# Kernel optimization log

Measured on AMD Instinct MI355X. Metric: run time of the kernel, lower is better.

Reference implementation:

```python
import jax, jax.numpy as jnp
import numpy as np

# dims
B, NO, NE = 32, 100, 600          # batch, img objects, img edges
NK, KE, L = 1000, 1000, 8         # kg entities, kg edges, token len
R = 8                              # reasoning-program nodes
H, IMG, LOC = 512, 2048, 5        # hidden, img feat, loc feat
EMB, V, MID, C = 300, 10000, 512, 3000
PAD = 1


def lang_encode(tokens, embed, W, b):
    # masked mean-pool of word embeddings + projection (LanguageEncoder)
    m = (tokens != PAD).astype(jnp.float32)            # [B,N,L]
    e = embed[tokens]                                   # [B,N,L,EMB]
    pooled = (e * m[..., None]).sum(-2) / jnp.maximum(m.sum(-1, keepdims=True), 1.0)
    return jnp.tanh(pooled @ W + b)                     # [B,N,H]


def find_attn(q, k, mask, Wq, Wk, v):
    # Find module: additive attention of program-node queries over key set
    qp = q @ Wq                                         # [B,R,MID]
    kp = k @ Wk                                         # [B,N,MID]
    s = jnp.einsum('brnm,m->brn', jnp.tanh(qp[:, :, None, :] + kp[:, None, :, :]), v)
    if mask is not None:
        s = jnp.where(mask[:, None, :], s, -1e9)
    return jax.nn.softmax(s, axis=-1)                   # [B,R,N] attention maps


def setup_inputs():
    key = jax.random.key(0)
    ks = jax.random.split(key, 30)
    w = lambda i, shp: jax.random.normal(ks[i], shp, jnp.float32) * 0.05
    inp = {
        'img_feat': jax.random.normal(ks[0], (B, NO, IMG), jnp.float32),
        'img_loc': jax.random.uniform(ks[1], (B, NO, LOC), jnp.float32),
        'img_node1_id_list': jax.random.randint(ks[2], (B, NE), 0, NO),
        'img_node2_id_list': jax.random.randint(ks[3], (B, NE), 0, NO),
        'kg_entity': jax.random.randint(ks[4], (B, NK, L), 0, V),
        'kg_e1_ids_list': jax.random.randint(ks[5], (B, KE), 0, NK),
        'kg_e2_ids_list': jax.random.randint(ks[6], (B, KE), 0, NK),
        'kg_edge': jax.random.randint(ks[7], (B, KE, L), 0, V),
        'r_nodes': jax.random.randint(ks[8], (B, R, L), 0, V),
        'r_connects': jax.random.randint(ks[9], (B, R), 0, R),
        'r_type': jax.random.randint(ks[10], (B, R), 0, 3),
        'embed': w(11, (V, EMB)),
        'W_lang': w(12, (EMB, H)), 'b_lang': jnp.zeros((H,), jnp.float32),
        'W_img': w(13, (IMG, H)), 'b_img': jnp.zeros((H,), jnp.float32),
        'W_loc': w(14, (LOC, H)), 'b_loc': jnp.zeros((H,), jnp.float32),
        'W_rel': w(15, (2 * H, H)), 'b_rel': jnp.zeros((H,), jnp.float32),
        'Wq_n': w(16, (H, MID)), 'Wk_n': w(17, (H, MID)), 'v_n': w(18, (MID,)),
        'Wq_e': w(19, (H, MID)), 'Wk_e': w(20, (H, MID)), 'v_e': w(21, (MID,)),
        'W1': w(22, (H, MID)), 'b1': jnp.zeros((MID,), jnp.float32),
        'W2': w(23, (MID, C)), 'b2': jnp.zeros((C,), jnp.float32),
    }
    return inp


def reference(img_feat, img_loc, img_node1_id_list, img_node2_id_list, kg_entity,
              kg_e1_ids_list, kg_e2_ids_list, kg_edge, r_nodes, r_connects, r_type,
              embed, W_lang, b_lang, W_img, b_img, W_loc, b_loc, W_rel, b_rel,
              Wq_n, Wk_n, v_n, Wq_e, Wk_e, v_e, W1, b1, W2, b2):
    # --- image graph features ---
    img_f = img_feat @ W_img + b_img                    # [B,NO,H]
    img_node_feat = img_f + (img_loc @ W_loc + b_loc)
    n1 = jnp.take_along_axis(img_f, img_node1_id_list[..., None], axis=1)  # [B,NE,H]
    n2 = jnp.take_along_axis(img_f, img_node2_id_list[..., None], axis=1)
    img_edge_feat = jnp.concatenate([n1, n2], -1) @ W_rel + b_rel          # [B,NE,H]
    # --- kg graph features ---
    kg_node_feat = lang_encode(kg_entity, embed, W_lang, b_lang)           # [B,NK,H]
    kg_node_mask = jnp.any(kg_entity != PAD, axis=-1)                      # [B,NK]
    kg_edge_feat = lang_encode(kg_edge, embed, W_lang, b_lang)             # [B,KE,H]
    # --- reasoning-program node features ---
    r_feat = lang_encode(r_nodes, embed, W_lang, b_lang)                   # [B,R,H]
    # --- Find over nodes (img + kg entities) ---
    node_keys = jnp.concatenate([img_node_feat, kg_node_feat], axis=1)     # [B,NO+NK,H]
    node_mask = jnp.concatenate([jnp.ones((B, NO), bool), kg_node_mask], axis=1)
    all_map = find_attn(r_feat, node_keys, node_mask, Wq_n, Wk_n, v_n)     # [B,R,NO+NK]
    node_re = jnp.einsum('brn,bnh->brh', all_map, node_keys)               # grounded node feats
    # --- Find over edges (img + kg relations) ---
    edge_keys = jnp.concatenate([img_edge_feat, kg_edge_feat], axis=1)     # [B,NE+KE,H]
    edge_map = find_attn(r_feat, edge_keys, None, Wq_e, Wk_e, v_e)
    edge_ctx = jnp.einsum('brn,bnh->brh', edge_map, edge_keys)
    # --- Reason head on root program node ---
    final = node_re[:, -1] + edge_ctx[:, -1]                               # [B,H]
    return jnp.tanh(final @ W1 + b1) @ W2 + b2                             # [B,C]
```

## Files before the change

### kernel.cpp

```cpp
#include <hip/hip_runtime.h>
#include <hip/hip_bf16.h>
#include <math.h>

#define B_   32
#define NO_  100
#define NE_  600
#define NK_  1000
#define KE_  1000
#define L_   8
#define R_   8
#define H_   512
#define IMG_ 2048
#define LOC_ 5
#define EMB_ 300
#define MID_ 512
#define C_   3000
#define PAD_ 1

#define NN_  (NO_ + NK_)
#define NEK_ (NE_ + KE_)

typedef __attribute__((ext_vector_type(8))) short bf16x8;
typedef __attribute__((ext_vector_type(4))) float f32x4;

__device__ __forceinline__ float4 ldf4(const float* p) { return *(const float4*)p; }

__device__ __forceinline__ float bf2f(short s) {
    unsigned u = ((unsigned)(unsigned short)s) << 16;
    float f; __builtin_memcpy(&f, &u, 4); return f;
}
__device__ __forceinline__ short f2bf(float f) {
    unsigned u; __builtin_memcpy(&u, &f, 4);
    u = (u + 0x7fffu + ((u >> 16) & 1u)) >> 16;
    return (short)u;
}

__global__ __launch_bounds__(256) void wprep_kernel(
    const float* __restrict__ W, short* __restrict__ Wp, int K, int KS)
{
    int idx = blockIdx.x * 256 + threadIdx.x;
    int total = 4 * KS * 4 * 128;
    if (idx >= total) return;
    int nl = idx & 127;
    int kg = (idx >> 7) & 3;
    int t  = idx >> 9;
    int ks = t % KS;
    int nb = t / KS;
    int n = nb * 128 + nl;
    short o[8];
#pragma unroll
    for (int j = 0; j < 8; ++j) {
        int k = ks * 32 + kg * 8 + j;
        o[j] = (k < K) ? f2bf(W[(long)k * H_ + n]) : (short)0;
    }
    *(uint4*)&Wp[(long)idx * 8] = *(uint4*)o;
}

__global__ __launch_bounds__(256) void cvt_bf16_kernel(
    const float* __restrict__ src, short* __restrict__ dst, long n)
{
    long i = ((long)blockIdx.x * 256 + threadIdx.x) * 8;
    if (i >= n) return;
    float4 a = ldf4(src + i), b = ldf4(src + i + 4);
    short o[8] = { f2bf(a.x), f2bf(a.y), f2bf(a.z), f2bf(a.w),
                   f2bf(b.x), f2bf(b.y), f2bf(b.z), f2bf(b.w) };
    *(uint4*)&dst[i] = *(uint4*)o;
}

template<int AV, int EP>
__global__ __launch_bounds__(256) void mfma_gemm_kernel(
    const short* __restrict__ A, int lda, const short* __restrict__ Wp, int KS,
    const int* __restrict__ id1, const int* __restrict__ id2,
    const short* __restrict__ Agather,
    const float* __restrict__ bias, const float* __restrict__ bias2,
    const float* __restrict__ loc, const float* __restrict__ Wloc,
    const float* __restrict__ qp, const float* __restrict__ vvec,
    short* __restrict__ out0, short* __restrict__ out1,
    float* __restrict__ sout, int Nrows, int Mtot)
{
    __shared__ __align__(16) short As[4096];
    __shared__ __align__(16) short Bs[4096];
    int tid = threadIdx.x;
    int m0 = blockIdx.x * 128, nb = blockIdx.y, n0 = nb * 128;
    int w = tid >> 6, l = tid & 63, wr = w >> 1, wc = w & 1;
    int sr = tid >> 1, sh = tid & 1;

    long arow_off = 0; int r1 = 0, r2 = 0;
    if (AV == 0) {
        arow_off = (long)(m0 + sr) * lda;
    } else {
        int i = m0 + sr;
        int b = i / NE_;
        r1 = b * NO_ + id1[i];
        r2 = b * NO_ + id2[i];
    }
    const short* wslab = Wp + (long)nb * KS * 4096;

    uint4 av0, av1, bv0, bv1;
    auto loadA = [&](int ks) {
        const short* p;
        if (AV == 0) p = A + arow_off + ks * 32 + sh * 16;
        else {
            int kk = ks * 32;
            int row = (kk < 512) ? r1 : r2;
            p = Agather + (long)row * 512 + (kk & 511) + sh * 16;
        }
        av0 = *(const uint4*)p;
        av1 = *(const uint4*)(p + 8);
    };
    auto loadB = [&](int ks) {
        const uint4* p = (const uint4*)(wslab + (long)ks * 4096 + tid * 16);
        bv0 = p[0]; bv1 = p[1];
    };

    f32x4 acc[4][4];
#pragma unroll
    for (int m = 0; m < 4; ++m)
#pragma unroll
        for (int n = 0; n < 4; ++n)
#pragma unroll
            for (int k = 0; k < 4; ++k) acc[m][n][k] = 0.f;

    int kg = l >> 4, li = l & 15;
    loadA(0); loadB(0);
    for (int ks = 0; ks < KS; ++ks) {
        __syncthreads();
        *(uint4*)&As[(sh * 2) * 1024 + sr * 8]     = av0;
        *(uint4*)&As[(sh * 2 + 1) * 1024 + sr * 8] = av1;
        *(uint4*)&Bs[tid * 16]     = bv0;
        *(uint4*)&Bs[tid * 16 + 8] = bv1;
        __syncthreads();
        if (ks + 1 < KS) { loadA(ks + 1); loadB(ks + 1); }
        bf16x8 af[4], bfr[4];
#pragma unroll
        for (int m = 0; m < 4; ++m)
            af[m] = *(const bf16x8*)&As[kg * 1024 + (wr * 64 + m * 16 + li) * 8];
#pragma unroll
        for (int n = 0; n < 4; ++n)
            bfr[n] = *(const bf16x8*)&Bs[kg * 1024 + (wc * 64 + n * 16 + li) * 8];
#pragma unroll
        for (int m = 0; m < 4; ++m)
#pragma unroll
            for (int n = 0; n < 4; ++n)
                acc[m][n] = __builtin_amdgcn_mfma_f32_16x16x32_bf16(af[m], bfr[n], acc[m][n], 0, 0, 0);
    }

    int jrow4 = (l >> 4) * 4;
    if (EP == 0) {
        float bi[4], bl[4], wl[4][5];
#pragma unroll
        for (int n = 0; n < 4; ++n) {
            int col = n0 + wc * 64 + n * 16 + li;
            bi[n] = bias[col]; bl[n] = bias2[col];
#pragma unroll
            for (int j5 = 0; j5 < 5; ++j5) wl[n][j5] = Wloc[j5 * H_ + col];
        }
#pragma unroll
        for (int m = 0; m < 4; ++m)
#pragma unroll
            for (int j = 0; j < 4; ++j) {
                int row = m0 + wr * 64 + m * 16 + jrow4 + j;
                int b = row / NO_, o = row - b * NO_;
                float lv[5];
#pragma unroll
                for (int j5 = 0; j5 < 5; ++j5) lv[j5] = loc[(long)row * 5 + j5];
#pragma unroll
                for (int n = 0; n < 4; ++n) {
                    int col = n0 + wc * 64 + n * 16 + li;
                    float val = acc[m][n][j] + bi[n];
                    out0[(long)row * H_ + col] = f2bf(val);
                    float nk = val + bl[n];
#pragma unroll
                    for (int j5 = 0; j5 < 5; ++j5) nk = fmaf(lv[j5], wl[n][j5], nk);
                    out1[((long)b * NN_ + o) * H_ + col] = f2bf(nk);
                }
            }
    } else if (EP == 1) {
        float bi[4];
#pragma unroll
        for (int n = 0; n < 4; ++n) bi[n] = bias[n0 + wc * 64 + n * 16 + li];
#pragma unroll
        for (int m = 0; m < 4; ++m)
#pragma unroll
            for (int j = 0; j < 4; ++j) {
                int row = m0 + wr * 64 + m * 16 + jrow4 + j;
                int b = row / NE_, e = row - b * NE_;
#pragma unroll
                for (int n = 0; n < 4; ++n) {
                    int col = n0 + wc * 64 + n * 16 + li;
                    out0[((long)b * NEK_ + e) * H_ + col] = f2bf(acc[m][n][j] + bi[n]);
                }
            }
    } else {
        float vv[4];
        int cols[4];
#pragma unroll
        for (int n = 0; n < 4; ++n) {
            cols[n] = n0 + wc * 64 + n * 16 + li;
            vv[n] = vvec[cols[n]];
        }
        int slot = nb * 2 + wc;
#pragma unroll
        for (int m = 0; m < 4; ++m)
#pragma unroll
            for (int j = 0; j < 4; ++j) {
                int row = m0 + wr * 64 + m * 16 + jrow4 + j;
                int b = row / Nrows;
                const float* qpb = qp + (long)b * H_;
                float p = 0.f;
#pragma unroll
                for (int n = 0; n < 4; ++n)
                    p += tanhf(qpb[cols[n]] + acc[m][n][j]) * vv[n];
                p += __shfl_xor(p, 1); p += __shfl_xor(p, 2);
                p += __shfl_xor(p, 4); p += __shfl_xor(p, 8);
                if (li == 0) sout[(long)slot * Mtot + row] = p;
            }
    }
}

template<int OUTF32>
__global__ __launch_bounds__(256) void lang_mfma_kernel(
    const int* __restrict__ tokens, int tok_stride, int tok_off,
    const float* __restrict__ embed, const short* __restrict__ Wp,
    const float* __restrict__ bias,
    void* __restrict__ out, int rows_per_b, long out_bstride, long out_roff,
    float* __restrict__ maskout, int nrows)
{
    __shared__ int   toks[32][8];
    __shared__ float rinv[32];
    __shared__ __align__(16) short Ap[40 * 32 * 8];
    __shared__ __align__(16) short Bs[4 * 4096];
    int tid = threadIdx.x;
    int base = blockIdx.x * 32;
    {
        int r = tid >> 3, tt = tid & 7;
        toks[r][tt] = tokens[tok_off + (long)(base + r) * tok_stride + tt];
    }
    __syncthreads();
    if (tid < 32) {
        int c = 0;
#pragma unroll
        for (int t = 0; t < 8; ++t) c += (toks[tid][t] != PAD_);
        rinv[tid] = 1.f / fmaxf((float)c, 1.f);
        if (maskout) maskout[base + tid] = (c > 0) ? 1.f : 0.f;
    }
    __syncthreads();

    for (int task = tid; task < 1280; task += 256) {
        int r = task / 40, kg = task - r * 40;
        float s[8] = {0.f,0.f,0.f,0.f,0.f,0.f,0.f,0.f};
        if (kg <= 37) {
#pragma unroll
            for (int t = 0; t < 8; ++t) {
                int tok = toks[r][t];
                if (tok != PAD_) {
                    const float* ep = embed + (long)tok * EMB_ + kg * 8;
                    float4 a = ldf4(ep);
                    s[0] += a.x; s[1] += a.y; s[2] += a.z; s[3] += a.w;
                    if (kg < 37) {
                        float4 b = ldf4(ep + 4);
                        s[4] += b.x; s[5] += b.y; s[6] += b.z; s[7] += b.w;
                    }
                }
            }
        }
        float iv = rinv[r];
        short o[8];
#pragma unroll
        for (int j = 0; j < 8; ++j) o[j] = f2bf(s[j] * iv);
        *(uint4*)&Ap[(kg * 32 + r) * 8] = *(uint4*)o;
    }

    int w = tid >> 6, l = tid & 63, kg = l >> 4, li = l & 15;
    f32x4 acc[2][8];
#pragma unroll
    for (int m = 0; m < 2; ++m)
#pragma unroll
        for (int n = 0; n < 8; ++n)
#pragma unroll
            for (int k = 0; k < 4; ++k) acc[m][n][k] = 0.f;

    for (int ks = 0; ks < 10; ++ks) {
        __syncthreads();
#pragma unroll
        for (int c = 0; c < 4; ++c) {
            int flat = c * 256 + tid;
            int nb = flat >> 8, rest = flat & 255;
            const uint4* p = (const uint4*)(Wp + (long)(nb * 10 + ks) * 4096 + rest * 16);
            uint4* q = (uint4*)&Bs[nb * 4096 + rest * 16];
            q[0] = p[0]; q[1] = p[1];
        }
        __syncthreads();
        bf16x8 af[2];
#pragma unroll
        for (int m = 0; m < 2; ++m)
            af[m] = *(const bf16x8*)&Ap[((ks * 4 + kg) * 32 + m * 16 + li) * 8];
#pragma unroll
        for (int n = 0; n < 8; ++n) {
            bf16x8 bf = *(const bf16x8*)&Bs[w * 4096 + kg * 1024 + (n * 16 + li) * 8];
#pragma unroll
            for (int m = 0; m < 2; ++m)
                acc[m][n] = __builtin_amdgcn_mfma_f32_16x16x32_bf16(af[m], bf, acc[m][n], 0, 0, 0);
        }
    }

#pragma unroll
    for (int m = 0; m < 2; ++m)
#pragma unroll
        for (int j = 0; j < 4; ++j) {
            int r = m * 16 + (l >> 4) * 4 + j;
            int i = base + r;
            if (i >= nrows) continue;
            int b = i / rows_per_b, k = i - b * rows_per_b;
#pragma unroll
            for (int n = 0; n < 8; ++n) {
                int col = w * 128 + n * 16 + li;
                float val = tanhf(acc[m][n][j] + bias[col]);
                long idx = (long)b * out_bstride + out_roff + (long)k * H_ + col;
                if (OUTF32) ((float*)out)[idx] = val;
                else        ((short*)out)[idx] = f2bf(val);
            }
        }
}

__global__ __launch_bounds__(256) void softmax_w_kernel(
    const float* __restrict__ sp_n, const float* __restrict__ sp_e,
    const float* __restrict__ maskbuf, float* __restrict__ wn, float* __restrict__ we)
{
    __shared__ float sw[NEK_];
    __shared__ float red[256];
    int b = blockIdx.x, tid = threadIdx.x, set = blockIdx.y;
    const float* sp = set ? sp_e : sp_n;
    float* wout = set ? we : wn;
    int N = set ? NEK_ : NN_;
    long Mtot = set ? (long)B_ * NEK_ : (long)B_ * NN_;

    float lmax = -3.0e38f;
    for (int n = tid; n < N; n += 256) {
        long row = (long)b * N + n;
        float x = 0.f;
#pragma unroll
        for (int s = 0; s < 8; ++s) x += sp[(long)s * Mtot + row];
        if (!set && n >= NO_ && maskbuf[(long)b * NK_ + (n - NO_)] == 0.f) x = -1e30f;
        sw[n] = x;
        lmax = fmaxf(lmax, x);
    }
    red[tid] = lmax; __syncthreads();
    for (int st = 128; st > 0; st >>= 1) {
        if (tid < st) red[tid] = fmaxf(red[tid], red[tid + st]);
        __syncthreads();
    }
    float mx = red[0]; __syncthreads();

    float lsum = 0.f;
    for (int n = tid; n < N; n += 256) {
        float e = expf(sw[n] - mx);
        sw[n] = e;
        lsum += e;
    }
    red[tid] = lsum; __syncthreads();
    for (int st = 128; st > 0; st >>= 1) {
        if (tid < st) red[tid] += red[tid + st];
        __syncthreads();
    }
    float invZ = 1.0f / red[0];
    __syncthreads();
    for (int n = tid; n < N; n += 256)
        wout[(long)b * N + n] = sw[n] * invZ;
}

template<int SP>
__global__ __launch_bounds__(256) void wsum_kernel(
    const float* __restrict__ w, const short* __restrict__ keys,
    float* __restrict__ partial, int N)
{
    __shared__ float red[4][512];
    int b = blockIdx.x, sp = blockIdx.y, tid = threadIdx.x;
    int c8 = (tid & 63) * 8, rsub = tid >> 6;
    int per = (N + SP - 1) / SP;
    int n0 = sp * per, n1 = min(n0 + per, N);
    float acc[8] = {0.f,0.f,0.f,0.f,0.f,0.f,0.f,0.f};
    for (int n = n0 + rsub; n < n1; n += 4) {
        float wv = w[(long)b * N + n];
        bf16x8 k = *(const bf16x8*)&keys[((long)b * N + n) * H_ + c8];
#pragma unroll
        for (int j = 0; j < 8; ++j) acc[j] = fmaf(wv, bf2f(k[j]), acc[j]);
    }
    *(float4*)&red[rsub][c8]     = *(float4*)acc;
    *(float4*)&red[rsub][c8 + 4] = *(float4*)(acc + 4);
    __syncthreads();
    if (rsub == 0) {
        float o[8];
#pragma unroll
        for (int j = 0; j < 8; ++j)
            o[j] = red[0][c8 + j] + red[1][c8 + j] + red[2][c8 + j] + red[3][c8 + j];
        float* op = &partial[((long)sp * B_ + b) * H_ + c8];
        *(float4*)op       = *(float4*)o;
        *(float4*)(op + 4) = *(float4*)(o + 4);
    }
}

__global__ __launch_bounds__(256) void fin_reduce_kernel(
    const float* __restrict__ pn, const float* __restrict__ pe, float* __restrict__ fin)
{
    int i = blockIdx.x * 256 + threadIdx.x;
    float s = 0.f;
#pragma unroll
    for (int sp = 0; sp < 16; ++sp)
        s += pn[(long)sp * B_ * H_ + i] + pe[(long)sp * B_ * H_ + i];
    fin[i] = s;
}

template<int E, int CHUNK>
__global__ __launch_bounds__(256) void kmatvec_kernel(
    const float* __restrict__ in, const float* __restrict__ Wa,
    const float* __restrict__ Wb, float* __restrict__ pa,
    float* __restrict__ pb, int C)
{
    __shared__ float ins[32 * CHUNK];
    int tid = threadIdx.x;
    int ks = blockIdx.y, k0 = ks * CHUNK;
    const float* W   = (blockIdx.z == 0) ? Wa : Wb;
    float* partial   = (blockIdx.z == 0) ? pa : pb;
    for (int t = tid; t < 32 * CHUNK; t += 256) {
        int b = t / CHUNK, k = t - b * CHUNK;
        ins[t] = in[(long)b * E + k0 + k];
    }
    __syncthreads();
    int c = blockIdx.x * 256 + tid;
    if (c >= C) return;
    float acc[32];
#pragma unroll
    for (int b = 0; b < 32; ++b) acc[b] = 0.f;
    for (int k = 0; k < CHUNK; ++k) {
        float wv = W[(long)(k0 + k) * C + c];
#pragma unroll
        for (int b = 0; b < 32; ++b)
            acc[b] = fmaf(ins[b * CHUNK + k], wv, acc[b]);
    }
#pragma unroll
    for (int b = 0; b < 32; ++b)
        partial[((long)ks * 32 + b) * C + c] = acc[b];
}

template<int ACT, int KS>
__global__ __launch_bounds__(256) void kreduce_kernel(
    const float* __restrict__ pa, const float* __restrict__ pb,
    const float* __restrict__ biasa, const float* __restrict__ biasb,
    float* __restrict__ oa, float* __restrict__ ob, int C)
{
    int set = blockIdx.y;
    const float* p    = set ? pb : pa;
    const float* bias = set ? biasb : biasa;
    float* o          = set ? ob : oa;
    long i = (long)blockIdx.x * 256 + threadIdx.x;
    if (i >= 32L * C) return;
    int c = (int)(i % C);
    float s = bias ? bias[c] : 0.f;
#pragma unroll
    for (int ks = 0; ks < KS; ++ks) s += p[(long)ks * 32 * C + i];
    o[i] = (ACT == 1) ? tanhf(s) : s;
}

extern "C" void kernel_launch(void* const* d_in, const int* in_sizes, int n_in,
                              void* d_out, int out_size, void* d_ws, size_t ws_size,
                              hipStream_t stream)
{
    (void)in_sizes; (void)n_in; (void)out_size; (void)ws_size;

    const float* img_feat  = (const float*)d_in[0];
    const float* img_loc   = (const float*)d_in[1];
    const int*   id1       = (const int*)d_in[2];
    const int*   id2       = (const int*)d_in[3];
    const int*   kg_entity = (const int*)d_in[4];
    const int*   kg_edge   = (const int*)d_in[7];
    const int*   r_nodes   = (const int*)d_in[8];
    const float* embed     = (const float*)d_in[11];
    const float* W_lang    = (const float*)d_in[12];
    const float* b_lang    = (const float*)d_in[13];
    const float* W_img     = (const float*)d_in[14];
    const float* b_img     = (const float*)d_in[15];
    const float* W_loc     = (const float*)d_in[16];
    const float* b_loc     = (const float*)d_in[17];
    const float* W_rel     = (const float*)d_in[18];
    const float* b_rel     = (const float*)d_in[19];
    const float* Wq_n      = (const float*)d_in[20];
    const float* Wk_n      = (const float*)d_in[21];
    const float* v_n       = (const float*)d_in[22];
    const float* Wq_e      = (const float*)d_in[23];
    const float* Wk_e      = (const float*)d_in[24];
    const float* v_e       = (const float*)d_in[25];
    const float* W1        = (const float*)d_in[26];
    const float* b1        = (const float*)d_in[27];
    const float* W2        = (const float*)d_in[28];
    const float* b2        = (const float*)d_in[29];
    float* out = (float*)d_out;

    char* ws = (char*)d_ws;
    size_t off = 0;
    auto allocS = [&](size_t n) { short* p = (short*)(ws + off); off += ((n * 2 + 255) & ~255ULL); return p; };
    auto allocF = [&](size_t n) { float* p = (float*)(ws + off); off += ((n * 4 + 255) & ~255ULL); return p; };

    short* img_feat_bf = allocS((size_t)B_ * NO_ * IMG_);
    short* Wp_img      = allocS((size_t)4 * 64 * 4096);
    short* Wp_rel      = allocS((size_t)4 * 32 * 4096);
    short* Wp_kn       = allocS((size_t)4 * 16 * 4096);
    short* Wp_ke       = allocS((size_t)4 * 16 * 4096);
    short* Wp_lang     = allocS((size_t)4 * 10 * 4096);
    short* img_f_bf    = allocS((size_t)B_ * NO_ * H_);
    short* node_keys   = allocS((size_t)B_ * NN_ * H_);
    short* edge_keys   = allocS((size_t)B_ * NEK_ * H_);
    float* rfeat   = allocF((size_t)B_ * H_);
    float* qp_n    = allocF((size_t)B_ * H_);
    float* qp_e    = allocF((size_t)B_ * H_);
    float* mask_kg = allocF((size_t)B_ * NK_);
    float* sp_n    = allocF((size_t)8 * B_ * NN_);
    float* sp_e    = allocF((size_t)8 * B_ * NEK_);
    float* wn      = allocF((size_t)B_ * NN_);
    float* we      = allocF((size_t)B_ * NEK_);
    float* pn      = allocF((size_t)16 * B_ * H_);
    float* pe      = allocF((size_t)16 * B_ * H_);
    float* fin     = allocF((size_t)B_ * H_);
    float* hid     = allocF((size_t)B_ * H_);
    float* pq_n    = allocF((size_t)16 * B_ * MID_);
    float* pq_e    = allocF((size_t)16 * B_ * MID_);
    float* ph1     = allocF((size_t)16 * B_ * MID_);
    float* ph2     = allocF((size_t)16 * B_ * C_);

    cvt_bf16_kernel<<<(B_ * NO_ * IMG_ / 8 + 255) / 256, 256, 0, stream>>>(
        img_feat, img_feat_bf, (long)B_ * NO_ * IMG_);
    wprep_kernel<<<512, 256, 0, stream>>>(W_img,  Wp_img,  IMG_, 64);
    wprep_kernel<<<256, 256, 0, stream>>>(W_rel,  Wp_rel,  1024, 32);
    wprep_kernel<<<128, 256, 0, stream>>>(Wk_n,   Wp_kn,   512,  16);
    wprep_kernel<<<128, 256, 0, stream>>>(Wk_e,   Wp_ke,   512,  16);
    wprep_kernel<<< 80, 256, 0, stream>>>(W_lang, Wp_lang, EMB_, 10);

    lang_mfma_kernel<1><<<1, 256, 0, stream>>>(
        r_nodes, R_ * L_, (R_ - 1) * L_, embed, Wp_lang, b_lang,
        rfeat, 1, (long)H_, 0L, nullptr, B_);
    lang_mfma_kernel<0><<<B_ * NK_ / 32, 256, 0, stream>>>(
        kg_entity, L_, 0, embed, Wp_lang, b_lang,
        node_keys, NK_, (long)NN_ * H_, (long)NO_ * H_, mask_kg, B_ * NK_);
    lang_mfma_kernel<0><<<B_ * KE_ / 32, 256, 0, stream>>>(
        kg_edge, L_, 0, embed, Wp_lang, b_lang,
        edge_keys, KE_, (long)NEK_ * H_, (long)NE_ * H_, nullptr, B_ * KE_);

    kmatvec_kernel<H_, 32><<<dim3(2, 16, 2), 256, 0, stream>>>(
        rfeat, Wq_n, Wq_e, pq_n, pq_e, MID_);
    kreduce_kernel<0, 16><<<dim3(B_ * MID_ / 256, 2), 256, 0, stream>>>(
        pq_n, pq_e, nullptr, nullptr, qp_n, qp_e, MID_);

    mfma_gemm_kernel<0, 0><<<dim3(B_ * NO_ / 128, 4), 256, 0, stream>>>(
        img_feat_bf, IMG_, Wp_img, 64, nullptr, nullptr, nullptr,
        b_img, b_loc, img_loc, W_loc, nullptr, nullptr,
        img_f_bf, node_keys, nullptr, 0, 0);
    mfma_gemm_kernel<2, 1><<<dim3(B_ * NE_ / 128, 4), 256, 0, stream>>>(
        nullptr, 0, Wp_rel, 32, id1, id2, img_f_bf,
        b_rel, nullptr, nullptr, nullptr, nullptr, nullptr,
        edge_keys, nullptr, nullptr, 0, 0);

    mfma_gemm_kernel<0, 2><<<dim3(B_ * NN_ / 128, 4), 256, 0, stream>>>(
        node_keys, H_, Wp_kn, 16, nullptr, nullptr, nullptr,
        nullptr, nullptr, nullptr, nullptr, qp_n, v_n,
        nullptr, nullptr, sp_n, NN_, B_ * NN_);
    mfma_gemm_kernel<0, 2><<<dim3(B_ * NEK_ / 128, 4), 256, 0, stream>>>(
        edge_keys, H_, Wp_ke, 16, nullptr, nullptr, nullptr,
        nullptr, nullptr, nullptr, nullptr, qp_e, v_e,
        nullptr, nullptr, sp_e, NEK_, B_ * NEK_);

    softmax_w_kernel<<<dim3(B_, 2), 256, 0, stream>>>(sp_n, sp_e, mask_kg, wn, we);
    wsum_kernel<16><<<dim3(B_, 16), 256, 0, stream>>>(wn, node_keys, pn, NN_);
    wsum_kernel<16><<<dim3(B_, 16), 256, 0, stream>>>(we, edge_keys, pe, NEK_);
    fin_reduce_kernel<<<B_ * H_ / 256, 256, 0, stream>>>(pn, pe, fin);

    kmatvec_kernel<H_, 32><<<dim3(2, 16, 1), 256, 0, stream>>>(
        fin, W1, W1, ph1, ph1, MID_);
    kreduce_kernel<1, 16><<<dim3(B_ * MID_ / 256, 1), 256, 0, stream>>>(
        ph1, ph1, b1, b1, hid, hid, MID_);
    kmatvec_kernel<MID_, 32><<<dim3((C_ + 255) / 256, 16, 1), 256, 0, stream>>>(
        hid, W2, W2, ph2, ph2, C_);
    kreduce_kernel<0, 16><<<dim3((B_ * C_ + 255) / 256, 1), 256, 0, stream>>>(
        ph2, ph2, b2, b2, out, out, C_);
}
```

Measured before the change: 512.4 us.

## Split language encoder into bf16 pooling pass and tiled MFMA keys GEMM

Replaces the fused per-32-row language encoder, which reloaded the full 512-column projection weight into shared memory for every 32-row block, with two stages. A pooling kernel gathers from a bf16 copy of the embedding table and writes padded pooled rows to a global buffer. A 128x128-tiled MFMA GEMM with register prefetch then projects those rows, so each weight tile serves four times as many rows. The cost is an extra global round trip for the pooled activations, an extra conversion pass over the embedding table, and bf16 rounding of embeddings before the mean.

```diff
diff --git a/kernel.cpp b/kernel.cpp
--- a/kernel.cpp
+++ b/kernel.cpp
@@ -65,6 +65,139 @@
     short o[8] = { f2bf(a.x), f2bf(a.y), f2bf(a.z), f2bf(a.w),
                    f2bf(b.x), f2bf(b.y), f2bf(b.z), f2bf(b.w) };
     *(uint4*)&dst[i] = *(uint4*)o;
+}
+
+__global__ __launch_bounds__(256) void pool_kernel(
+    const int* __restrict__ tokens, int tok_stride, int tok_off,
+    const short* __restrict__ embed_bf, short* __restrict__ pooled,
+    float* __restrict__ maskout, int nrows)
+{
+    __shared__ int   toks[32][8];
+    __shared__ float rinv[32];
+    int tid = threadIdx.x, base = blockIdx.x * 32;
+    {
+        int r = tid >> 3, t = tid & 7;
+        int i = base + r;
+        toks[r][t] = (i < nrows) ? tokens[tok_off + (long)i * tok_stride + t] : PAD_;
+    }
+    __syncthreads();
+    if (tid < 32) {
+        int c = 0;
+#pragma unroll
+        for (int t = 0; t < 8; ++t) c += (toks[tid][t] != PAD_);
+        rinv[tid] = 1.0f / fmaxf((float)c, 1.0f);
+        int i = base + tid;
+        if (maskout && i < nrows) maskout[i] = (c > 0) ? 1.0f : 0.0f;
+    }
+    __syncthreads();
+
+    for (int task = tid; task < 32 * 40; task += 256) {
+        int r = task / 40, kg = task - r * 40;
+        float s[8] = {0.f,0.f,0.f,0.f,0.f,0.f,0.f,0.f};
+        if (kg < 38) {
+#pragma unroll
+            for (int t = 0; t < 8; ++t) {
+                int tok = toks[r][t];
+                if (tok != PAD_) {
+                    bf16x8 e = *(const bf16x8*)&embed_bf[(long)tok * EMB_ + kg * 8];
+#pragma unroll
+                    for (int j = 0; j < 8; ++j) s[j] += bf2f(e[j]);
+                }
+            }
+        }
+        float iv = rinv[r];
+        short o[8];
+#pragma unroll
+        for (int j = 0; j < 8; ++j) {
+            float v = s[j] * iv;
+            if (kg == 37 && j >= 4) v = 0.f;
+            o[j] = f2bf(v);
+        }
+        *(uint4*)&pooled[(long)(base + r) * 320 + kg * 8] = *(uint4*)o;
+    }
+}
+
+template<int OUTF32>
+__global__ __launch_bounds__(256) void keys_gemm_kernel(
+    const short* __restrict__ A, const short* __restrict__ Wp,
+    const float* __restrict__ bias,
+    void* __restrict__ out, int rows_per_b, long out_bstride, long out_roff,
+    float* __restrict__ unused, int nrows)
+{
+    const int KS = 10;
+    __shared__ __align__(16) short As[4096];
+    __shared__ __align__(16) short Bs[4096];
+    int tid = threadIdx.x;
+    int m0 = blockIdx.x * 128, nb = blockIdx.y, n0 = nb * 128;
+    int w = tid >> 6, l = tid & 63, wr = w >> 1, wc = w & 1;
+    int sr = tid >> 1, sh = tid & 1;
+    long arow_off = (long)(m0 + sr) * 320;
+    const short* wslab = Wp + (long)nb * KS * 4096;
+
+    uint4 av0, av1, bv0, bv1;
+    auto loadA = [&](int ks) {
+        const short* p = A + arow_off + ks * 32 + sh * 16;
+        av0 = *(const uint4*)p;
+        av1 = *(const uint4*)(p + 8);
+    };
+    auto loadB = [&](int ks) {
+        const uint4* p = (const uint4*)(wslab + (long)ks * 4096 + tid * 16);
+        bv0 = p[0]; bv1 = p[1];
+    };
+
+    f32x4 acc[4][4];
+#pragma unroll
+    for (int m = 0; m < 4; ++m)
+#pragma unroll
+        for (int n = 0; n < 4; ++n)
+#pragma unroll
+            for (int k = 0; k < 4; ++k) acc[m][n][k] = 0.f;
+
+    int kg = l >> 4, li = l & 15;
+    loadA(0); loadB(0);
+    for (int ks = 0; ks < KS; ++ks) {
+        __syncthreads();
+        *(uint4*)&As[(sh * 2) * 1024 + sr * 8]     = av0;
+        *(uint4*)&As[(sh * 2 + 1) * 1024 + sr * 8] = av1;
+        *(uint4*)&Bs[tid * 16]     = bv0;
+        *(uint4*)&Bs[tid * 16 + 8] = bv1;
+        __syncthreads();
+        if (ks + 1 < KS) { loadA(ks + 1); loadB(ks + 1); }
+        bf16x8 af[4], bfr[4];
+#pragma unroll
+        for (int m = 0; m < 4; ++m)
+            af[m] = *(const bf16x8*)&As[kg * 1024 + (wr * 64 + m * 16 + li) * 8];
+#pragma unroll
+        for (int n = 0; n < 4; ++n)
+            bfr[n] = *(const bf16x8*)&Bs[kg * 1024 + (wc * 64 + n * 16 + li) * 8];
+#pragma unroll
+        for (int m = 0; m < 4; ++m)
+#pragma unroll
+            for (int n = 0; n < 4; ++n)
+                acc[m][n] = __builtin_amdgcn_mfma_f32_16x16x32_bf16(af[m], bfr[n], acc[m][n], 0, 0, 0);
+    }
+
+    int jrow4 = (l >> 4) * 4;
+    float bv[4];
+#pragma unroll
+    for (int n = 0; n < 4; ++n) bv[n] = bias[n0 + wc * 64 + n * 16 + li];
+#pragma unroll
+    for (int m = 0; m < 4; ++m)
+#pragma unroll
+        for (int j = 0; j < 4; ++j) {
+            int i = m0 + wr * 64 + m * 16 + jrow4 + j;
+            if (i >= nrows) continue;
+            int b = i / rows_per_b, k = i - b * rows_per_b;
+#pragma unroll
+            for (int n = 0; n < 4; ++n) {
+                int col = n0 + wc * 64 + n * 16 + li;
+                float val = tanhf(acc[m][n][j] + bv[n]);
+                long idx = (long)b * out_bstride + out_roff + (long)k * H_ + col;
+                if (OUTF32) ((float*)out)[idx] = val;
+                else        ((short*)out)[idx] = f2bf(val);
+            }
+        }
+    (void)unused;
 }
 
 template<int AV, int EP>
@@ -216,111 +349,6 @@
                 if (li == 0) sout[(long)slot * Mtot + row] = p;
             }
     }
-}
-
-template<int OUTF32>
-__global__ __launch_bounds__(256) void lang_mfma_kernel(
-    const int* __restrict__ tokens, int tok_stride, int tok_off,
-    const float* __restrict__ embed, const short* __restrict__ Wp,
-    const float* __restrict__ bias,
-    void* __restrict__ out, int rows_per_b, long out_bstride, long out_roff,
-    float* __restrict__ maskout, int nrows)
-{
-    __shared__ int   toks[32][8];
-    __shared__ float rinv[32];
-    __shared__ __align__(16) short Ap[40 * 32 * 8];
-    __shared__ __align__(16) short Bs[4 * 4096];
-    int tid = threadIdx.x;
-    int base = blockIdx.x * 32;
-    {
-        int r = tid >> 3, tt = tid & 7;
-        toks[r][tt] = tokens[tok_off + (long)(base + r) * tok_stride + tt];
-    }
-    __syncthreads();
-    if (tid < 32) {
-        int c = 0;
-#pragma unroll
-        for (int t = 0; t < 8; ++t) c += (toks[tid][t] != PAD_);
-        rinv[tid] = 1.f / fmaxf((float)c, 1.f);
-        if (maskout) maskout[base + tid] = (c > 0) ? 1.f : 0.f;
-    }
-    __syncthreads();
-
-    for (int task = tid; task < 1280; task += 256) {
-        int r = task / 40, kg = task - r * 40;
-        float s[8] = {0.f,0.f,0.f,0.f,0.f,0.f,0.f,0.f};
-        if (kg <= 37) {
-#pragma unroll
-            for (int t = 0; t < 8; ++t) {
-                int tok = toks[r][t];
-                if (tok != PAD_) {
-                    const float* ep = embed + (long)tok * EMB_ + kg * 8;
-                    float4 a = ldf4(ep);
-                    s[0] += a.x; s[1] += a.y; s[2] += a.z; s[3] += a.w;
-                    if (kg < 37) {
-                        float4 b = ldf4(ep + 4);
-                        s[4] += b.x; s[5] += b.y; s[6] += b.z; s[7] += b.w;
-                    }
-                }
-            }
-        }
-        float iv = rinv[r];
-        short o[8];
-#pragma unroll
-        for (int j = 0; j < 8; ++j) o[j] = f2bf(s[j] * iv);
-        *(uint4*)&Ap[(kg * 32 + r) * 8] = *(uint4*)o;
-    }
-
-    int w = tid >> 6, l = tid & 63, kg = l >> 4, li = l & 15;
-    f32x4 acc[2][8];
-#pragma unroll
-    for (int m = 0; m < 2; ++m)
-#pragma unroll
-        for (int n = 0; n < 8; ++n)
-#pragma unroll
-            for (int k = 0; k < 4; ++k) acc[m][n][k] = 0.f;
-
-    for (int ks = 0; ks < 10; ++ks) {
-        __syncthreads();
-#pragma unroll
-        for (int c = 0; c < 4; ++c) {
-            int flat = c * 256 + tid;
-            int nb = flat >> 8, rest = flat & 255;
-            const uint4* p = (const uint4*)(Wp + (long)(nb * 10 + ks) * 4096 + rest * 16);
-            uint4* q = (uint4*)&Bs[nb * 4096 + rest * 16];
-            q[0] = p[0]; q[1] = p[1];
-        }
-        __syncthreads();
-        bf16x8 af[2];
-#pragma unroll
-        for (int m = 0; m < 2; ++m)
-            af[m] = *(const bf16x8*)&Ap[((ks * 4 + kg) * 32 + m * 16 + li) * 8];
-#pragma unroll
-        for (int n = 0; n < 8; ++n) {
-            bf16x8 bf = *(const bf16x8*)&Bs[w * 4096 + kg * 1024 + (n * 16 + li) * 8];
-#pragma unroll
-            for (int m = 0; m < 2; ++m)
-                acc[m][n] = __builtin_amdgcn_mfma_f32_16x16x32_bf16(af[m], bf, acc[m][n], 0, 0, 0);
-        }
-    }
-
-#pragma unroll
-    for (int m = 0; m < 2; ++m)
-#pragma unroll
-        for (int j = 0; j < 4; ++j) {
-            int r = m * 16 + (l >> 4) * 4 + j;
-            int i = base + r;
-            if (i >= nrows) continue;
-            int b = i / rows_per_b, k = i - b * rows_per_b;
-#pragma unroll
-            for (int n = 0; n < 8; ++n) {
-                int col = w * 128 + n * 16 + li;
-                float val = tanhf(acc[m][n][j] + bias[col]);
-                long idx = (long)b * out_bstride + out_roff + (long)k * H_ + col;
-                if (OUTF32) ((float*)out)[idx] = val;
-                else        ((short*)out)[idx] = f2bf(val);
-            }
-        }
 }
 
 __global__ __launch_bounds__(256) void softmax_w_kernel(
@@ -502,6 +530,7 @@
     auto allocF = [&](size_t n) { float* p = (float*)(ws + off); off += ((n * 4 + 255) & ~255ULL); return p; };
 
     short* img_feat_bf = allocS((size_t)B_ * NO_ * IMG_);
+    short* embed_bf    = allocS((size_t)10000 * EMB_ + 16);
     short* Wp_img      = allocS((size_t)4 * 64 * 4096);
     short* Wp_rel      = allocS((size_t)4 * 32 * 4096);
     short* Wp_kn       = allocS((size_t)4 * 16 * 4096);
@@ -510,6 +539,9 @@
     short* img_f_bf    = allocS((size_t)B_ * NO_ * H_);
     short* node_keys   = allocS((size_t)B_ * NN_ * H_);
     short* edge_keys   = allocS((size_t)B_ * NEK_ * H_);
+    short* pooled_n    = allocS((size_t)B_ * NK_ * 320);
+    short* pooled_e    = allocS((size_t)B_ * KE_ * 320);
+    short* pooled_r    = allocS((size_t)128 * 320);
     float* rfeat   = allocF((size_t)B_ * H_);
     float* qp_n    = allocF((size_t)B_ * H_);
     float* qp_e    = allocF((size_t)B_ * H_);
@@ -529,21 +561,29 @@
 
     cvt_bf16_kernel<<<(B_ * NO_ * IMG_ / 8 + 255) / 256, 256, 0, stream>>>(
         img_feat, img_feat_bf, (long)B_ * NO_ * IMG_);
+    cvt_bf16_kernel<<<(10000 * EMB_ / 8 + 255) / 256, 256, 0, stream>>>(
+        embed, embed_bf, (long)10000 * EMB_);
     wprep_kernel<<<512, 256, 0, stream>>>(W_img,  Wp_img,  IMG_, 64);
     wprep_kernel<<<256, 256, 0, stream>>>(W_rel,  Wp_rel,  1024, 32);
     wprep_kernel<<<128, 256, 0, stream>>>(Wk_n,   Wp_kn,   512,  16);
     wprep_kernel<<<128, 256, 0, stream>>>(Wk_e,   Wp_ke,   512,  16);
     wprep_kernel<<< 80, 256, 0, stream>>>(W_lang, Wp_lang, EMB_, 10);
 
-    lang_mfma_kernel<1><<<1, 256, 0, stream>>>(
-        r_nodes, R_ * L_, (R_ - 1) * L_, embed, Wp_lang, b_lang,
-        rfeat, 1, (long)H_, 0L, nullptr, B_);
-    lang_mfma_kernel<0><<<B_ * NK_ / 32, 256, 0, stream>>>(
-        kg_entity, L_, 0, embed, Wp_lang, b_lang,
-        node_keys, NK_, (long)NN_ * H_, (long)NO_ * H_, mask_kg, B_ * NK_);
-    lang_mfma_kernel<0><<<B_ * KE_ / 32, 256, 0, stream>>>(
-        kg_edge, L_, 0, embed, Wp_lang, b_lang,
-        edge_keys, KE_, (long)NEK_ * H_, (long)NE_ * H_, nullptr, B_ * KE_);
+    pool_kernel<<<B_ * NK_ / 32, 256, 0, stream>>>(
+        kg_entity, L_, 0, embed_bf, pooled_n, mask_kg, B_ * NK_);
+    pool_kernel<<<B_ * KE_ / 32, 256, 0, stream>>>(
+        kg_edge, L_, 0, embed_bf, pooled_e, nullptr, B_ * KE_);
+    pool_kernel<<<4, 256, 0, stream>>>(
+        r_nodes, R_ * L_, (R_ - 1) * L_, embed_bf, pooled_r, nullptr, B_);
+
+    keys_gemm_kernel<0><<<dim3(B_ * NK_ / 128, 4), 256, 0, stream>>>(
+        pooled_n, Wp_lang, b_lang, node_keys, NK_, (long)NN_ * H_, (long)NO_ * H_,
+        nullptr, B_ * NK_);
+    keys_gemm_kernel<0><<<dim3(B_ * KE_ / 128, 4), 256, 0, stream>>>(
+        pooled_e, Wp_lang, b_lang, edge_keys, KE_, (long)NEK_ * H_, (long)NE_ * H_,
+        nullptr, B_ * KE_);
+    keys_gemm_kernel<1><<<dim3(1, 4), 256, 0, stream>>>(
+        pooled_r, Wp_lang, b_lang, rfeat, 1, (long)H_, 0L, nullptr, B_);
 
     kmatvec_kernel<H_, 32><<<dim3(2, 16, 2), 256, 0, stream>>>(
         rfeat, Wq_n, Wq_e, pq_n, pq_e, MID_);
```

Result: faster. 447.1 us (-12.8%).
